# Optimization experiments

Hardware: AMD Instinct MI355X
Metric: run time of the kernel (lower is better)

Reference implementation:

```python
import jax, jax.numpy as jnp
import numpy as np

EPS = 1e-5

def setup_inputs() -> dict:
    key = jax.random.key(0)
    ks = jax.random.split(key, 12)
    B = 4096
    x = jax.random.normal(ks[0], (B, 28, 28, 1), dtype=jnp.float32)
    # BatchNorm1d(1) affine params (applied per-channel over active sites)
    bn_gamma = jnp.ones((1,), jnp.float32)
    bn_beta = jnp.zeros((1,), jnp.float32)
    # SubMConv2d weights, HWIO layout
    w1 = jax.random.normal(ks[1], (3, 3, 1, 32), jnp.float32) * 0.1
    b1 = jax.random.normal(ks[2], (32,), jnp.float32) * 0.01
    w2 = jax.random.normal(ks[3], (3, 3, 32, 64), jnp.float32) * 0.05
    b2 = jax.random.normal(ks[4], (64,), jnp.float32) * 0.01
    # FC layers (torch Linear: y = x @ W.T + b)
    fcw1 = jax.random.normal(ks[5], (128, 14 * 14 * 64), jnp.float32) * 0.01
    fcb1 = jnp.zeros((128,), jnp.float32)
    fcw2 = jax.random.normal(ks[6], (10, 128), jnp.float32) * 0.05
    fcb2 = jnp.zeros((10,), jnp.float32)
    return {"x": x, "bn_gamma": bn_gamma, "bn_beta": bn_beta,
            "w1": w1, "b1": b1, "w2": w2, "b2": b2,
            "fcw1": fcw1, "fcb1": fcb1, "fcw2": fcw2, "fcb2": fcb2}

def _subm_conv(feat, mask, w, b):
    # Submanifold conv: inactive inputs are zero (already masked), and the
    # output coordinate set equals the input active set -> mask the output.
    y = jax.lax.conv_general_dilated(
        feat, w, window_strides=(1, 1), padding='SAME',
        dimension_numbers=('NHWC', 'HWIO', 'NHWC'))
    return jnp.where(mask, y + b, 0.0)

def reference(x, bn_gamma, bn_beta, w1, b1, w2, b2, fcw1, fcb1, fcw2, fcb2):
    # from_dense: active sites are locations with nonzero feature. [B,28,28,1]
    mask = (x != 0)  # single channel -> site mask [B,28,28,1]
    maskf = mask.astype(x.dtype)
    # BatchNorm1d(1) on the [N_active, 1] sparse feature tensor (batch stats)
    n = jnp.maximum(maskf.sum(), 1.0)
    mean = (x * maskf).sum() / n
    var = (jnp.square(x - mean) * maskf).sum() / n
    feat = maskf * (bn_gamma * (x - mean) * jax.lax.rsqrt(var + EPS) + bn_beta)
    # SubMConv2d(1,32,3,1) + ReLU
    h = jax.nn.relu(_subm_conv(feat, mask, w1, b1))  # [B,28,28,32]
    # SubMConv2d(32,64,3,1) + ReLU
    h = jax.nn.relu(_subm_conv(h, mask, w2, b2))     # [B,28,28,64]
    # SparseMaxPool2d(2,2): max over active sites per window; since values are
    # post-ReLU (>=0) and inactive sites hold 0, dense maxpool is exact, and
    # fully-inactive windows correctly yield 0 after ToDense.
    h = jax.lax.reduce_window(h, -jnp.inf, jax.lax.max,
                              (1, 2, 2, 1), (1, 2, 2, 1), 'VALID')  # [B,14,14,64]
    # ToDense gives NCHW [B,64,14,14]; torch.flatten uses C-major order
    h = jnp.transpose(h, (0, 3, 1, 2)).reshape(h.shape[0], -1)  # [B,12544]
    # dropout1/dropout2 are identity in eval mode
    h = jax.nn.relu(h @ fcw1.T + fcb1)
    logits = h @ fcw2.T + fcb2
    return jax.nn.log_softmax(logits, axis=1)
```

## Files before the change

kernel.cpp:

```cpp
#include <hip/hip_runtime.h>
#include <stdint.h>

typedef unsigned short u16;
typedef unsigned int u32;
typedef __attribute__((ext_vector_type(8))) short bf16x8;
typedef __attribute__((ext_vector_type(4))) float f32x4;

__device__ __forceinline__ u16 f2bf(float f) {
    u32 u = __float_as_uint(f);
    u32 r = (u + 0x7fffu + ((u >> 16) & 1u)) >> 16;
    return (u16)r;
}

__device__ __forceinline__ u32 cvtpk(float lo, float hi) {
    u32 r;
    asm("v_cvt_pk_bf16_f32 %0, %1, %2" : "=v"(r) : "v"(lo), "v"(hi));
    return r;
}

__device__ __forceinline__ void gload16(const u16* src, u16* dst) {
    __builtin_amdgcn_global_load_lds(
        (const __attribute__((address_space(1))) u32*)src,
        (__attribute__((address_space(3))) u32*)dst, 16, 0, 0);
}

__global__ __launch_bounds__(256) void k_stats(const float* __restrict__ x, int n,
                                               float* __restrict__ stats) {
    int t = blockIdx.x * 256 + threadIdx.x;
    int stride = gridDim.x * 256;
    float c = 0.f, s = 0.f, ss = 0.f;
    for (int i = t; i < n; i += stride) {
        float v = x[i];
        if (v != 0.f) { c += 1.f; s += v; ss = fmaf(v, v, ss); }
    }
    for (int off = 32; off > 0; off >>= 1) {
        c  += __shfl_down(c, off);
        s  += __shfl_down(s, off);
        ss += __shfl_down(ss, off);
    }
    __shared__ float red[3][4];
    int lane = threadIdx.x & 63, wv = threadIdx.x >> 6;
    if (lane == 0) { red[0][wv] = c; red[1][wv] = s; red[2][wv] = ss; }
    __syncthreads();
    if (threadIdx.x == 0) {
        atomicAdd(&stats[0], red[0][0] + red[0][1] + red[0][2] + red[0][3]);
        atomicAdd(&stats[1], red[1][0] + red[1][1] + red[1][2] + red[1][3]);
        atomicAdd(&stats[2], red[2][0] + red[2][1] + red[2][2] + red[2][3]);
    }
}

__global__ void k_finalize(const float* __restrict__ g, const float* __restrict__ b,
                           float* __restrict__ stats) {
    float n = stats[0]; if (n < 1.f) n = 1.f;
    float mean = stats[1] / n;
    float var = stats[2] / n - mean * mean;
    if (var < 0.f) var = 0.f;
    float scale = g[0] * rsqrtf(var + 1e-5f);
    stats[4] = scale;
    stats[5] = b[0] - mean * scale;
}

__global__ __launch_bounds__(256) void k_prepall(const float* __restrict__ w2,
    const float* __restrict__ fcw1, u16* __restrict__ w2b, u16* __restrict__ fcw1b, int n)
{
    int i = blockIdx.x * 256 + threadIdx.x;
    if (i < 9 * 64 * 32) {
        int tap = i >> 11, rem = i & 2047, co = rem >> 5, ci = rem & 31;
        w2b[i] = f2bf(w2[tap * 2048 + ci * 64 + co]);
    }
    if (i < n) fcw1b[i] = f2bf(fcw1[i]);
}

__global__ __launch_bounds__(256, 4) void k_conv1(const float* __restrict__ x,
    const float* __restrict__ w1, const float* __restrict__ b1,
    const float* __restrict__ stats, u16* __restrict__ h1g,
    unsigned char* __restrict__ pmg)
{
    __shared__ float feat[30][30];
    __shared__ unsigned char mk[784];
    const int t = threadIdx.x;
    const int b = blockIdx.x;
    const float scale = stats[4], shift = stats[5];

    for (int i = t; i < 900; i += 256) (&feat[0][0])[i] = 0.f;
    __syncthreads();
    const float* xb = x + (size_t)b * 784;
    for (int i = t; i < 784; i += 256) {
        float v = xb[i];
        bool m = (v != 0.f);
        mk[i] = m ? 1 : 0;
        int h = i / 28, w = i - h * 28;
        feat[h + 1][w + 1] = m ? fmaf(v, scale, shift) : 0.f;
    }
    __syncthreads();

    u16* hb_img = h1g + (size_t)b * 28928;

    if (t < 196) {
        int rr = t / 14, cc = t - rr * 14;
        int base = rr * 56 + cc * 2;
        pmg[(size_t)b * 200 + t] = (unsigned char)(mk[base] | (mk[base + 1] << 1)
              | (mk[base + 28] << 2) | (mk[base + 29] << 3));
    }
    if (t < 120) {
        int slot;
        if (t < 30)       slot = t;
        else if (t < 60)  slot = 840 + t;
        else if (t < 88)  slot = (t - 59) * 30;
        else if (t < 116) slot = (t - 87) * 30 + 29;
        else              slot = 784 + t;
        const uint4 z = make_uint4(0u, 0u, 0u, 0u);
        #pragma unroll
        for (int g = 0; g < 4; ++g)
            *(uint4*)&hb_img[g * 7232 + slot * 8] = z;
    }

    const int cp = (t >> 4) & 3;
    const int pxg = (t & 15) | ((t >> 6) << 4);
    float wk[9][8], bs[8];
    {
        float4 b0 = *(const float4*)(b1 + cp * 8);
        float4 b4 = *(const float4*)(b1 + cp * 8 + 4);
        bs[0]=b0.x; bs[1]=b0.y; bs[2]=b0.z; bs[3]=b0.w;
        bs[4]=b4.x; bs[5]=b4.y; bs[6]=b4.z; bs[7]=b4.w;
    }
    #pragma unroll
    for (int j = 0; j < 9; ++j) {
        float4 w0 = *(const float4*)(w1 + j * 32 + cp * 8);
        float4 w4 = *(const float4*)(w1 + j * 32 + cp * 8 + 4);
        wk[j][0]=w0.x; wk[j][1]=w0.y; wk[j][2]=w0.z; wk[j][3]=w0.w;
        wk[j][4]=w4.x; wk[j][5]=w4.y; wk[j][6]=w4.z; wk[j][7]=w4.w;
    }
    u16* hb = hb_img + cp * 7232;
    for (int px = pxg; px < 784; px += 64) {
        int h = px / 28, w = px - h * 28;
        float a[8];
        #pragma unroll
        for (int c = 0; c < 8; ++c) a[c] = bs[c];
        #pragma unroll
        for (int kh = 0; kh < 3; ++kh)
            #pragma unroll
            for (int kw = 0; kw < 3; ++kw) {
                float f = feat[h + kh][w + kw];
                #pragma unroll
                for (int c = 0; c < 8; ++c) a[c] = fmaf(f, wk[kh * 3 + kw][c], a[c]);
            }
        float mf = mk[px] ? 1.f : 0.f;
        u32 q0 = cvtpk(fmaxf(a[0], 0.f) * mf, fmaxf(a[1], 0.f) * mf);
        u32 q1 = cvtpk(fmaxf(a[2], 0.f) * mf, fmaxf(a[3], 0.f) * mf);
        u32 q2 = cvtpk(fmaxf(a[4], 0.f) * mf, fmaxf(a[5], 0.f) * mf);
        u32 q3 = cvtpk(fmaxf(a[6], 0.f) * mf, fmaxf(a[7], 0.f) * mf);
        *(uint4*)&hb[((h + 1) * 30 + (w + 1)) * 8] = make_uint4(q0, q1, q2, q3);
    }
}

__global__ __launch_bounds__(256, 2) void k_conv2(const u16* __restrict__ h1g,
    const unsigned char* __restrict__ pmg, const u16* __restrict__ w2b,
    const float* __restrict__ b2, u16* __restrict__ pooled)
{
    __shared__ u16 h1[28928];
    __shared__ unsigned char pm[200];
    const int t = threadIdx.x;
    const int b = blockIdx.x;
    const int lane = t & 63;
    const int wv = t >> 6;
    const int lg = lane >> 4;
    const int lr = lane & 15;

    const u16* src = h1g + (size_t)b * 28928;
    #pragma unroll
    for (int i = 0; i < 14; ++i)
        gload16(src + (i * 256 + t) * 8, &h1[(i * 256 + t) * 8]);
    if (t < 32) {
        uint4 v = *(const uint4*)(src + (3584 + t) * 8);
        *(uint4*)&h1[(3584 + t) * 8] = v;
    }
    if (t < 50) ((u32*)pm)[t] = ((const u32*)(pmg + (size_t)b * 200))[t];

    bf16x8 wf[9][4];
    #pragma unroll
    for (int tap = 0; tap < 9; ++tap)
        #pragma unroll
        for (int nt = 0; nt < 4; ++nt)
            wf[tap][nt] = *(const bf16x8*)(w2b + tap * 2048 + (nt * 16 + lr) * 32 + lg * 8);
    float bias2[4];
    #pragma unroll
    for (int nt = 0; nt < 4; ++nt) bias2[nt] = b2[nt * 16 + lr];

    asm volatile("s_waitcnt vmcnt(0)" ::: "memory");
    __syncthreads();

    const int cb = wv & 1;
    const int r0 = wv >> 1;
    const char* gb = (const char*)h1 + lg * 14464 + (cb * 16 + lr) * 16;
    const bool store_ok = !(cb == 1 && lg == 3);
    const int pc0 = cb * 8 + lg * 2;
    u16* poolb = pooled + (size_t)b * 12544;

    #pragma unroll 1
    for (int i = 0; i < 7; ++i) {
        const int r = r0 + 2 * i;
        const char* ab = gb + 960 * r;
        bf16x8 a0[3], a1[3], a2[3], a3[3];
        #pragma unroll
        for (int kw = 0; kw < 3; ++kw) {
            a0[kw] = *(const bf16x8*)(ab + kw * 16);
            a1[kw] = *(const bf16x8*)(ab + 480 + kw * 16);
            a2[kw] = *(const bf16x8*)(ab + 960 + kw * 16);
        }
        f32x4 acc0[4], acc1[4];
        #pragma unroll
        for (int nt = 0; nt < 4; ++nt) {
            acc0[nt] = (f32x4){bias2[nt], bias2[nt], bias2[nt], bias2[nt]};
            acc1[nt] = acc0[nt];
        }
        #pragma unroll
        for (int nt = 0; nt < 4; ++nt)
            #pragma unroll
            for (int kw = 0; kw < 3; ++kw) {
                acc0[nt] = __builtin_amdgcn_mfma_f32_16x16x32_bf16(a0[kw], wf[kw][nt], acc0[nt], 0, 0, 0);
                acc0[nt] = __builtin_amdgcn_mfma_f32_16x16x32_bf16(a1[kw], wf[3 + kw][nt], acc0[nt], 0, 0, 0);
                acc0[nt] = __builtin_amdgcn_mfma_f32_16x16x32_bf16(a2[kw], wf[6 + kw][nt], acc0[nt], 0, 0, 0);
            }
        #pragma unroll
        for (int kw = 0; kw < 3; ++kw)
            a3[kw] = *(const bf16x8*)(ab + 1440 + kw * 16);
        #pragma unroll
        for (int nt = 0; nt < 4; ++nt)
            #pragma unroll
            for (int kw = 0; kw < 3; ++kw) {
                acc1[nt] = __builtin_amdgcn_mfma_f32_16x16x32_bf16(a1[kw], wf[kw][nt], acc1[nt], 0, 0, 0);
                acc1[nt] = __builtin_amdgcn_mfma_f32_16x16x32_bf16(a2[kw], wf[3 + kw][nt], acc1[nt], 0, 0, 0);
                acc1[nt] = __builtin_amdgcn_mfma_f32_16x16x32_bf16(a3[kw], wf[6 + kw][nt], acc1[nt], 0, 0, 0);
            }

        if (store_ok) {
            u32 pmw = *(const u16*)&pm[r * 14 + pc0];
            float m00 = (pmw & 1u)    ? 1.f : 0.f, m01 = (pmw & 2u)    ? 1.f : 0.f;
            float m10 = (pmw & 4u)    ? 1.f : 0.f, m11 = (pmw & 8u)    ? 1.f : 0.f;
            float n00 = (pmw & 256u)  ? 1.f : 0.f, n01 = (pmw & 512u)  ? 1.f : 0.f;
            float n10 = (pmw & 1024u) ? 1.f : 0.f, n11 = (pmw & 2048u) ? 1.f : 0.f;
            #pragma unroll
            for (int nt = 0; nt < 4; ++nt) {
                float p0 = fmaxf(fmaxf(fmaxf(acc0[nt][0], 0.f) * m00, fmaxf(acc0[nt][1], 0.f) * m01),
                                 fmaxf(fmaxf(acc1[nt][0], 0.f) * m10, fmaxf(acc1[nt][1], 0.f) * m11));
                float p1 = fmaxf(fmaxf(fmaxf(acc0[nt][2], 0.f) * n00, fmaxf(acc0[nt][3], 0.f) * n01),
                                 fmaxf(fmaxf(acc1[nt][2], 0.f) * n10, fmaxf(acc1[nt][3], 0.f) * n11));
                *(u32*)&poolb[(nt * 16 + lr) * 196 + r * 14 + pc0] =
                    (u32)f2bf(p0) | ((u32)f2bf(p1) << 16);
            }
        }
    }
}

__global__ __launch_bounds__(256, 2) void k_conv(const float* __restrict__ x,
    const float* __restrict__ w1, const float* __restrict__ b1,
    const u16* __restrict__ w2b, const float* __restrict__ b2,
    const float* __restrict__ stats, u16* __restrict__ pooled)
{
    __shared__ u16 h1[28928];
    __shared__ float feat[30][30];
    __shared__ unsigned char mk[784];
    __shared__ unsigned char pm[200];
    const int t = threadIdx.x;
    const int b = blockIdx.x;
    const int lane = t & 63;
    const int wv = t >> 6;
    const int lg = lane >> 4;
    const int lr = lane & 15;

    const float scale = stats[4], shift = stats[5];

    for (int i = t; i < 14464; i += 256) ((u32*)h1)[i] = 0u;
    for (int i = t; i < 900; i += 256) (&feat[0][0])[i] = 0.f;
    __syncthreads();

    const float* xb = x + (size_t)b * 784;
    for (int i = t; i < 784; i += 256) {
        float v = xb[i];
        bool m = (v != 0.f);
        mk[i] = m ? 1 : 0;
        int h = i / 28, w = i - h * 28;
        feat[h + 1][w + 1] = m ? fmaf(v, scale, shift) : 0.f;
    }
    __syncthreads();

    if (t < 196) {
        int rr = t / 14, cc = t - rr * 14;
        int base = rr * 56 + cc * 2;
        pm[t] = (unsigned char)(mk[base] | (mk[base + 1] << 1)
              | (mk[base + 28] << 2) | (mk[base + 29] << 3));
    }

    {
        const int cp = (t >> 4) & 3;
        const int pxg = (t & 15) | ((t >> 6) << 4);
        float wk[9][8], bs[8];
        {
            float4 b0 = *(const float4*)(b1 + cp * 8);
            float4 b4 = *(const float4*)(b1 + cp * 8 + 4);
            bs[0]=b0.x; bs[1]=b0.y; bs[2]=b0.z; bs[3]=b0.w;
            bs[4]=b4.x; bs[5]=b4.y; bs[6]=b4.z; bs[7]=b4.w;
        }
        #pragma unroll
        for (int j = 0; j < 9; ++j) {
            float4 w0 = *(const float4*)(w1 + j * 32 + cp * 8);
            float4 w4 = *(const float4*)(w1 + j * 32 + cp * 8 + 4);
            wk[j][0]=w0.x; wk[j][1]=w0.y; wk[j][2]=w0.z; wk[j][3]=w0.w;
            wk[j][4]=w4.x; wk[j][5]=w4.y; wk[j][6]=w4.z; wk[j][7]=w4.w;
        }
        char* hb = (char*)h1 + cp * 14464;
        for (int px = pxg; px < 784; px += 64) {
            if (!mk[px]) continue;
            int h = px / 28, w = px - h * 28;
            float a[8];
            #pragma unroll
            for (int c = 0; c < 8; ++c) a[c] = bs[c];
            #pragma unroll
            for (int kh = 0; kh < 3; ++kh)
                #pragma unroll
                for (int kw = 0; kw < 3; ++kw) {
                    float f = feat[h + kh][w + kw];
                    #pragma unroll
                    for (int c = 0; c < 8; ++c) a[c] = fmaf(f, wk[kh * 3 + kw][c], a[c]);
                }
            u32 q0 = (u32)f2bf(fmaxf(a[0], 0.f)) | ((u32)f2bf(fmaxf(a[1], 0.f)) << 16);
            u32 q1 = (u32)f2bf(fmaxf(a[2], 0.f)) | ((u32)f2bf(fmaxf(a[3], 0.f)) << 16);
            u32 q2 = (u32)f2bf(fmaxf(a[4], 0.f)) | ((u32)f2bf(fmaxf(a[5], 0.f)) << 16);
            u32 q3 = (u32)f2bf(fmaxf(a[6], 0.f)) | ((u32)f2bf(fmaxf(a[7], 0.f)) << 16);
            *(uint4*)(hb + ((h + 1) * 30 + (w + 1)) * 16) = make_uint4(q0, q1, q2, q3);
        }
    }
    __syncthreads();

    bf16x8 wf[9][4];
    #pragma unroll
    for (int tap = 0; tap < 9; ++tap)
        #pragma unroll
        for (int nt = 0; nt < 4; ++nt)
            wf[tap][nt] = *(const bf16x8*)(w2b + tap * 2048 + (nt * 16 + lr) * 32 + lg * 8);
    float bias2[4];
    #pragma unroll
    for (int nt = 0; nt < 4; ++nt) bias2[nt] = b2[nt * 16 + lr];

    const int cb = wv & 1;
    const int r0 = wv >> 1;
    const char* gb = (const char*)h1 + lg * 14464 + (cb * 16 + lr) * 16;
    const bool store_ok = !(cb == 1 && lg == 3);
    const int pc0 = cb * 8 + lg * 2;
    u16* poolb = pooled + (size_t)b * 12544;

    #pragma unroll 1
    for (int i = 0; i < 7; ++i) {
        const int r = r0 + 2 * i;
        const char* ab = gb + 960 * r;
        bf16x8 a0[3], a1[3], a2[3], a3[3];
        #pragma unroll
        for (int kw = 0; kw < 3; ++kw) {
            a0[kw] = *(const bf16x8*)(ab + kw * 16);
            a1[kw] = *(const bf16x8*)(ab + 480 + kw * 16);
            a2[kw] = *(const bf16x8*)(ab + 960 + kw * 16);
        }
        f32x4 acc0[4], acc1[4];
        #pragma unroll
        for (int nt = 0; nt < 4; ++nt) {
            acc0[nt] = (f32x4){bias2[nt], bias2[nt], bias2[nt], bias2[nt]};
            acc1[nt] = acc0[nt];
        }
        #pragma unroll
        for (int nt = 0; nt < 4; ++nt)
            #pragma unroll
            for (int kw = 0; kw < 3; ++kw) {
                acc0[nt] = __builtin_amdgcn_mfma_f32_16x16x32_bf16(a0[kw], wf[kw][nt], acc0[nt], 0, 0, 0);
                acc0[nt] = __builtin_amdgcn_mfma_f32_16x16x32_bf16(a1[kw], wf[3 + kw][nt], acc0[nt], 0, 0, 0);
                acc0[nt] = __builtin_amdgcn_mfma_f32_16x16x32_bf16(a2[kw], wf[6 + kw][nt], acc0[nt], 0, 0, 0);
            }
        #pragma unroll
        for (int kw = 0; kw < 3; ++kw)
            a3[kw] = *(const bf16x8*)(ab + 1440 + kw * 16);
        #pragma unroll
        for (int nt = 0; nt < 4; ++nt)
            #pragma unroll
            for (int kw = 0; kw < 3; ++kw) {
                acc1[nt] = __builtin_amdgcn_mfma_f32_16x16x32_bf16(a1[kw], wf[kw][nt], acc1[nt], 0, 0, 0);
                acc1[nt] = __builtin_amdgcn_mfma_f32_16x16x32_bf16(a2[kw], wf[3 + kw][nt], acc1[nt], 0, 0, 0);
                acc1[nt] = __builtin_amdgcn_mfma_f32_16x16x32_bf16(a3[kw], wf[6 + kw][nt], acc1[nt], 0, 0, 0);
            }

        if (store_ok) {
            u32 pmw = *(const u16*)&pm[r * 14 + pc0];
            float m00 = (pmw & 1u)    ? 1.f : 0.f, m01 = (pmw & 2u)    ? 1.f : 0.f;
            float m10 = (pmw & 4u)    ? 1.f : 0.f, m11 = (pmw & 8u)    ? 1.f : 0.f;
            float n00 = (pmw & 256u)  ? 1.f : 0.f, n01 = (pmw & 512u)  ? 1.f : 0.f;
            float n10 = (pmw & 1024u) ? 1.f : 0.f, n11 = (pmw & 2048u) ? 1.f : 0.f;
            #pragma unroll
            for (int nt = 0; nt < 4; ++nt) {
                float p0 = fmaxf(fmaxf(fmaxf(acc0[nt][0], 0.f) * m00, fmaxf(acc0[nt][1], 0.f) * m01),
                                 fmaxf(fmaxf(acc1[nt][0], 0.f) * m10, fmaxf(acc1[nt][1], 0.f) * m11));
                float p1 = fmaxf(fmaxf(fmaxf(acc0[nt][2], 0.f) * n00, fmaxf(acc0[nt][3], 0.f) * n01),
                                 fmaxf(fmaxf(acc1[nt][2], 0.f) * n10, fmaxf(acc1[nt][3], 0.f) * n11));
                *(u32*)&poolb[(nt * 16 + lr) * 196 + r * 14 + pc0] =
                    (u32)f2bf(p0) | ((u32)f2bf(p1) << 16);
            }
        }
    }
}

__global__ __launch_bounds__(256, 4) void k_fc1(const u16* __restrict__ pooled,
    const u16* __restrict__ fcw1b, float* __restrict__ fc1, int M)
{
    __shared__ u16 Asm[8 * 64 * 8];
    __shared__ u16 Bsm[8 * 128 * 8];
    const int t = threadIdx.x;
    const int m0 = blockIdx.x * 64;
    const int kbase = blockIdx.y * 1792;
    const int lane = t & 63;
    const int wv = t >> 6;
    const int lg = lane >> 4, lr = lane & 15;
    const int wm = wv & 1, wn = wv >> 1;

    const int ia0 = t, ia1 = t + 256;
    const u16* as0 = pooled + (size_t)(m0 + (ia0 & 63)) * 12544 + (ia0 >> 6) * 8 + kbase;
    const u16* as1 = pooled + (size_t)(m0 + (ia1 & 63)) * 12544 + (ia1 >> 6) * 8 + kbase;
    const u16* bs0 = fcw1b + (size_t)(t & 127) * 12544 + ((t >> 7) + 0) * 8 + kbase;
    const u16* bs1 = fcw1b + (size_t)(t & 127) * 12544 + ((t >> 7) + 2) * 8 + kbase;
    const u16* bs2 = fcw1b + (size_t)(t & 127) * 12544 + ((t >> 7) + 4) * 8 + kbase;
    const u16* bs3 = fcw1b + (size_t)(t & 127) * 12544 + ((t >> 7) + 6) * 8 + kbase;
    u16* ad0 = &Asm[(size_t)ia0 * 8];
    u16* ad1 = &Asm[(size_t)ia1 * 8];
    u16* bd0 = &Bsm[(size_t)(t + 0) * 8];
    u16* bd1 = &Bsm[(size_t)(t + 256) * 8];
    u16* bd2 = &Bsm[(size_t)(t + 512) * 8];
    u16* bd3 = &Bsm[(size_t)(t + 768) * 8];

    f32x4 acc[2][4];
    #pragma unroll
    for (int mi = 0; mi < 2; ++mi)
        #pragma unroll
        for (int ni = 0; ni < 4; ++ni) acc[mi][ni] = (f32x4){0.f, 0.f, 0.f, 0.f};

    for (int s = 0; s < 28; ++s) {
        const int kk = s * 64;
        __syncthreads();
        gload16(as0 + kk, ad0);
        gload16(as1 + kk, ad1);
        gload16(bs0 + kk, bd0);
        gload16(bs1 + kk, bd1);
        gload16(bs2 + kk, bd2);
        gload16(bs3 + kk, bd3);
        asm volatile("s_waitcnt vmcnt(0)" ::: "memory");
        __syncthreads();
        #pragma unroll
        for (int ks = 0; ks < 2; ++ks) {
            bf16x8 a[2], bfr[4];
            #pragma unroll
            for (int mi = 0; mi < 2; ++mi)
                a[mi] = *(const bf16x8*)&Asm[(((ks * 4 + lg) * 64) + wm * 32 + mi * 16 + lr) * 8];
            #pragma unroll
            for (int ni = 0; ni < 4; ++ni)
                bfr[ni] = *(const bf16x8*)&Bsm[(((ks * 4 + lg) * 128) + wn * 64 + ni * 16 + lr) * 8];
            #pragma unroll
            for (int mi = 0; mi < 2; ++mi)
                #pragma unroll
                for (int ni = 0; ni < 4; ++ni)
                    acc[mi][ni] = __builtin_amdgcn_mfma_f32_16x16x32_bf16(a[mi], bfr[ni], acc[mi][ni], 0, 0, 0);
        }
    }

    #pragma unroll
    for (int mi = 0; mi < 2; ++mi)
        #pragma unroll
        for (int ni = 0; ni < 4; ++ni)
            #pragma unroll
            for (int q = 0; q < 4; ++q) {
                int m = m0 + wm * 32 + mi * 16 + lg * 4 + q;
                int n = wn * 64 + ni * 16 + lr;
                atomicAdd(&fc1[(size_t)m * 128 + n], acc[mi][ni][q]);
            }
}

__global__ __launch_bounds__(256) void k_fc2(const float* __restrict__ fc1,
    const float* __restrict__ fcb1, const float* __restrict__ fcw2,
    const float* __restrict__ fcb2, float* __restrict__ out, int M)
{
    __shared__ float red[8][32][10];
    const int t = threadIdx.x;
    const int ml = t & 31, kq = t >> 5;
    const int m = blockIdx.x * 32 + ml;
    float acc[10];
    #pragma unroll
    for (int c = 0; c < 10; ++c) acc[c] = 0.f;
    const float* fp = fc1 + (size_t)m * 128 + kq * 16;
    #pragma unroll
    for (int j = 0; j < 16; j += 4) {
        float4 v4 = *(const float4*)(fp + j);
        float vv[4] = {v4.x, v4.y, v4.z, v4.w};
        #pragma unroll
        for (int u = 0; u < 4; ++u) {
            int k = kq * 16 + j + u;
            float v = fmaxf(vv[u] + fcb1[k], 0.f);
            #pragma unroll
            for (int c = 0; c < 10; ++c) acc[c] = fmaf(v, fcw2[c * 128 + k], acc[c]);
        }
    }
    #pragma unroll
    for (int c = 0; c < 10; ++c) red[kq][ml][c] = acc[c];
    __syncthreads();
    if (kq == 0) {
        float lgt[10];
        #pragma unroll
        for (int c = 0; c < 10; ++c) {
            float sv = 0.f;
            #pragma unroll
            for (int s = 0; s < 8; ++s) sv += red[s][ml][c];
            lgt[c] = sv + fcb2[c];
        }
        float mx = lgt[0];
        #pragma unroll
        for (int c = 1; c < 10; ++c) mx = fmaxf(mx, lgt[c]);
        float se = 0.f;
        #pragma unroll
        for (int c = 0; c < 10; ++c) se += expf(lgt[c] - mx);
        float lse = mx + logf(se);
        #pragma unroll
        for (int c = 0; c < 10; ++c) out[(size_t)m * 10 + c] = lgt[c] - lse;
    }
}

extern "C" void kernel_launch(void* const* d_in, const int* in_sizes, int n_in,
                              void* d_out, int out_size, void* d_ws, size_t ws_size,
                              hipStream_t stream) {
    const float* x     = (const float*)d_in[0];
    const float* gamma = (const float*)d_in[1];
    const float* beta  = (const float*)d_in[2];
    const float* w1    = (const float*)d_in[3];
    const float* b1    = (const float*)d_in[4];
    const float* w2    = (const float*)d_in[5];
    const float* b2    = (const float*)d_in[6];
    const float* fcw1  = (const float*)d_in[7];
    const float* fcb1  = (const float*)d_in[8];
    const float* fcw2  = (const float*)d_in[9];
    const float* fcb2  = (const float*)d_in[10];
    float* out = (float*)d_out;

    const int B = in_sizes[0] / 784;

    char* base = (char*)d_ws;
    float* stats  = (float*)base;
    u16*   w2b    = (u16*)(base + 256);
    float* fc1    = (float*)(base + 256);
    size_t off_pooled = 256 + (size_t)B * 128 * 4;
    u16*   pooled = (u16*)(base + off_pooled);
    size_t off_fcw1b = off_pooled + (size_t)B * 12544 * 2;
    u16*   fcw1b  = (u16*)(base + off_fcw1b);
    size_t off_pmg = off_fcw1b + (size_t)128 * 12544 * 2;
    unsigned char* pmg = (unsigned char*)(base + off_pmg);
    size_t off_h1g = off_pmg + (size_t)B * 200;
    u16*   h1g    = (u16*)(base + off_h1g);
    size_t need_split = off_h1g + (size_t)B * 57856;

    hipMemsetAsync(stats, 0, 32, stream);
    k_stats<<<1024, 256, 0, stream>>>(x, B * 784, stats);
    k_finalize<<<1, 1, 0, stream>>>(gamma, beta, stats);
    k_prepall<<<(128 * 12544 + 255) / 256, 256, 0, stream>>>(w2, fcw1, w2b, fcw1b, 128 * 12544);

    if (ws_size >= need_split) {
        k_conv1<<<B, 256, 0, stream>>>(x, w1, b1, stats, h1g, pmg);
        k_conv2<<<B, 256, 0, stream>>>(h1g, pmg, w2b, b2, pooled);
    } else {
        k_conv<<<B, 256, 0, stream>>>(x, w1, b1, w2b, b2, stats, pooled);
    }

    hipMemsetAsync(fc1, 0, (size_t)B * 128 * 4, stream);
    k_fc1<<<dim3(B / 64, 7), 256, 0, stream>>>(pooled, fcw1b, fc1, B);
    k_fc2<<<B / 32, 256, 0, stream>>>(fc1, fcb1, fcw2, fcb2, out, B);
}
```

Measured before the change: 354.1 us.

## Chunk split conv path to reuse h1 buffer, zero only halo, use cvt_pk

The split conv1/conv2 path now runs in batch chunks that share one reusable h1 global buffer. Chunk size comes from the available workspace, so the split path can run in smaller workspaces, and the h1 scratch stays smaller and more cache-resident. In the fused kernel, only the halo border of the h1 LDS tile is zeroed rather than the whole tile. Inactive pixels are no longer skipped; they are computed and multiplied by the mask, which removes divergence but adds arithmetic. Manual bf16 rounding is replaced with the v_cvt_pk_bf16_f32 instruction, and the extra launches per chunk add some overhead.

Measured after the change: 388.9 us. 9.8% more time.

```diff
diff --git a/kernel.cpp b/kernel.cpp
--- a/kernel.cpp
+++ b/kernel.cpp
@@ -246,8 +246,7 @@
                                  fmaxf(fmaxf(acc1[nt][0], 0.f) * m10, fmaxf(acc1[nt][1], 0.f) * m11));
                 float p1 = fmaxf(fmaxf(fmaxf(acc0[nt][2], 0.f) * n00, fmaxf(acc0[nt][3], 0.f) * n01),
                                  fmaxf(fmaxf(acc1[nt][2], 0.f) * n10, fmaxf(acc1[nt][3], 0.f) * n11));
-                *(u32*)&poolb[(nt * 16 + lr) * 196 + r * 14 + pc0] =
-                    (u32)f2bf(p0) | ((u32)f2bf(p1) << 16);
+                *(u32*)&poolb[(nt * 16 + lr) * 196 + r * 14 + pc0] = cvtpk(p0, p1);
             }
         }
     }
@@ -271,8 +270,19 @@
 
     const float scale = stats[4], shift = stats[5];
 
-    for (int i = t; i < 14464; i += 256) ((u32*)h1)[i] = 0u;
     for (int i = t; i < 900; i += 256) (&feat[0][0])[i] = 0.f;
+    if (t < 120) {
+        int slot;
+        if (t < 30)       slot = t;
+        else if (t < 60)  slot = 840 + t;
+        else if (t < 88)  slot = (t - 59) * 30;
+        else if (t < 116) slot = (t - 87) * 30 + 29;
+        else              slot = 784 + t;
+        const uint4 z = make_uint4(0u, 0u, 0u, 0u);
+        #pragma unroll
+        for (int g = 0; g < 4; ++g)
+            *(uint4*)&h1[g * 7232 + slot * 8] = z;
+    }
     __syncthreads();
 
     const float* xb = x + (size_t)b * 784;
@@ -311,7 +321,6 @@
         }
         char* hb = (char*)h1 + cp * 14464;
         for (int px = pxg; px < 784; px += 64) {
-            if (!mk[px]) continue;
             int h = px / 28, w = px - h * 28;
             float a[8];
             #pragma unroll
@@ -324,10 +333,11 @@
                     #pragma unroll
                     for (int c = 0; c < 8; ++c) a[c] = fmaf(f, wk[kh * 3 + kw][c], a[c]);
                 }
-            u32 q0 = (u32)f2bf(fmaxf(a[0], 0.f)) | ((u32)f2bf(fmaxf(a[1], 0.f)) << 16);
-            u32 q1 = (u32)f2bf(fmaxf(a[2], 0.f)) | ((u32)f2bf(fmaxf(a[3], 0.f)) << 16);
-            u32 q2 = (u32)f2bf(fmaxf(a[4], 0.f)) | ((u32)f2bf(fmaxf(a[5], 0.f)) << 16);
-            u32 q3 = (u32)f2bf(fmaxf(a[6], 0.f)) | ((u32)f2bf(fmaxf(a[7], 0.f)) << 16);
+            float mf = mk[px] ? 1.f : 0.f;
+            u32 q0 = cvtpk(fmaxf(a[0], 0.f) * mf, fmaxf(a[1], 0.f) * mf);
+            u32 q1 = cvtpk(fmaxf(a[2], 0.f) * mf, fmaxf(a[3], 0.f) * mf);
+            u32 q2 = cvtpk(fmaxf(a[4], 0.f) * mf, fmaxf(a[5], 0.f) * mf);
+            u32 q3 = cvtpk(fmaxf(a[6], 0.f) * mf, fmaxf(a[7], 0.f) * mf);
             *(uint4*)(hb + ((h + 1) * 30 + (w + 1)) * 16) = make_uint4(q0, q1, q2, q3);
         }
     }
@@ -399,8 +409,7 @@
                                  fmaxf(fmaxf(acc1[nt][0], 0.f) * m10, fmaxf(acc1[nt][1], 0.f) * m11));
                 float p1 = fmaxf(fmaxf(fmaxf(acc0[nt][2], 0.f) * n00, fmaxf(acc0[nt][3], 0.f) * n01),
                                  fmaxf(fmaxf(acc1[nt][2], 0.f) * n10, fmaxf(acc1[nt][3], 0.f) * n11));
-                *(u32*)&poolb[(nt * 16 + lr) * 196 + r * 14 + pc0] =
-                    (u32)f2bf(p0) | ((u32)f2bf(p1) << 16);
+                *(u32*)&poolb[(nt * 16 + lr) * 196 + r * 14 + pc0] = cvtpk(p0, p1);
             }
         }
     }
@@ -544,34 +553,51 @@
     float* out = (float*)d_out;
 
     const int B = in_sizes[0] / 784;
-
     char* base = (char*)d_ws;
-    float* stats  = (float*)base;
-    u16*   w2b    = (u16*)(base + 256);
-    float* fc1    = (float*)(base + 256);
-    size_t off_pooled = 256 + (size_t)B * 128 * 4;
-    u16*   pooled = (u16*)(base + off_pooled);
-    size_t off_fcw1b = off_pooled + (size_t)B * 12544 * 2;
-    u16*   fcw1b  = (u16*)(base + off_fcw1b);
-    size_t off_pmg = off_fcw1b + (size_t)128 * 12544 * 2;
-    unsigned char* pmg = (unsigned char*)(base + off_pmg);
-    size_t off_h1g = off_pmg + (size_t)B * 200;
-    u16*   h1g    = (u16*)(base + off_h1g);
-    size_t need_split = off_h1g + (size_t)B * 57856;
+    float* stats = (float*)base;
+
+    const size_t o_w2b = 256;
+    const size_t o_pmg = 37376;
+    const size_t o_r1  = o_pmg + (size_t)B * 200;
+    const size_t tail  = (size_t)B * 25088 + (size_t)128 * 25088;
+    long long avail = (long long)ws_size - (long long)(o_r1 + tail);
+    int CH = avail > 0 ? (int)(avail / 57856) : 0;
+    if (CH > B) CH = B;
+    const bool use_split = (CH >= 512);
 
     hipMemsetAsync(stats, 0, 32, stream);
     k_stats<<<1024, 256, 0, stream>>>(x, B * 784, stats);
     k_finalize<<<1, 1, 0, stream>>>(gamma, beta, stats);
-    k_prepall<<<(128 * 12544 + 255) / 256, 256, 0, stream>>>(w2, fcw1, w2b, fcw1b, 128 * 12544);
-
-    if (ws_size >= need_split) {
-        k_conv1<<<B, 256, 0, stream>>>(x, w1, b1, stats, h1g, pmg);
-        k_conv2<<<B, 256, 0, stream>>>(h1g, pmg, w2b, b2, pooled);
+
+    if (use_split) {
+        u16* w2b = (u16*)(base + o_w2b);
+        unsigned char* pmg = (unsigned char*)(base + o_pmg);
+        u16* h1g = (u16*)(base + o_r1);
+        float* fc1 = (float*)(base + o_r1);
+        u16* pooled = (u16*)(base + o_r1 + (size_t)CH * 57856);
+        u16* fcw1b = (u16*)((char*)pooled + (size_t)B * 25088);
+
+        k_prepall<<<(128 * 12544 + 255) / 256, 256, 0, stream>>>(w2, fcw1, w2b, fcw1b, 128 * 12544);
+        for (int c0 = 0; c0 < B; c0 += CH) {
+            int nb = (B - c0 < CH) ? (B - c0) : CH;
+            k_conv1<<<nb, 256, 0, stream>>>(x + (size_t)c0 * 784, w1, b1, stats,
+                                            h1g, pmg + (size_t)c0 * 200);
+            k_conv2<<<nb, 256, 0, stream>>>(h1g, pmg + (size_t)c0 * 200, w2b, b2,
+                                            pooled + (size_t)c0 * 12544);
+        }
+        hipMemsetAsync(fc1, 0, (size_t)B * 128 * 4, stream);
+        k_fc1<<<dim3(B / 64, 7), 256, 0, stream>>>(pooled, fcw1b, fc1, B);
+        k_fc2<<<B / 32, 256, 0, stream>>>(fc1, fcb1, fcw2, fcb2, out, B);
     } else {
+        u16* w2b = (u16*)(base + 256);
+        float* fc1 = (float*)(base + 256);
+        u16* pooled = (u16*)(base + 256 + (size_t)B * 512);
+        u16* fcw1b = (u16*)(base + 256 + (size_t)B * 512 + (size_t)B * 25088);
+
+        k_prepall<<<(128 * 12544 + 255) / 256, 256, 0, stream>>>(w2, fcw1, w2b, fcw1b, 128 * 12544);
         k_conv<<<B, 256, 0, stream>>>(x, w1, b1, w2b, b2, stats, pooled);
-    }
-
-    hipMemsetAsync(fc1, 0, (size_t)B * 128 * 4, stream);
-    k_fc1<<<dim3(B / 64, 7), 256, 0, stream>>>(pooled, fcw1b, fc1, B);
-    k_fc2<<<B / 32, 256, 0, stream>>>(fc1, fcb1, fcw2, fcb2, out, B);
-}
+        hipMemsetAsync(fc1, 0, (size_t)B * 128 * 4, stream);
+        k_fc1<<<dim3(B / 64, 7), 256, 0, stream>>>(pooled, fcw1b, fc1, B);
+        k_fc2<<<B / 32, 256, 0, stream>>>(fc1, fcb1, fcw2, fcb2, out, B);
+    }
+}
```
